# Performance work log

Hardware: AMD Instinct MI355X
Metric: run time of the kernel (lower is better)

The kernel has to match this reference:

```python
import jax, jax.numpy as jnp
import numpy as np

B, S, E, H = 4, 2048, 2048, 16
HD = E // H  # 128
SCALE = 1.0 / float(np.sqrt(HD))


def setup_inputs() -> dict:
    key = jax.random.key(0)
    ks = jax.random.split(key, 9)
    std = 0.02
    return {
        "QKV": jax.random.normal(ks[0], (B, S, E), dtype=jnp.float32),
        "Wq": jax.random.normal(ks[1], (E, E), dtype=jnp.float32) * std,
        "bq": jnp.zeros((E,), dtype=jnp.float32),
        "Wk": jax.random.normal(ks[2], (E, E), dtype=jnp.float32) * std,
        "bk": jnp.zeros((E,), dtype=jnp.float32),
        "Wv": jax.random.normal(ks[3], (E, E), dtype=jnp.float32) * std,
        "bv": jnp.zeros((E,), dtype=jnp.float32),
        "Wo": jax.random.normal(ks[4], (E, E), dtype=jnp.float32) * std,
        "bo": jnp.zeros((E,), dtype=jnp.float32),
        "is_causal": 1,
    }


def _split_heads(x):
    # [B,S,E] -> [B,H,S,HD]
    return x.reshape(B, -1, H, HD).transpose(0, 2, 1, 3)


def reference(QKV, Wq, bq, Wk, bk, Wv, bv, Wo, bo, is_causal):
    # nn.Linear: y = x @ W.T + b
    Q = _split_heads(QKV @ Wq.T + bq)
    K = _split_heads(QKV @ Wk.T + bk)
    V = _split_heads(QKV @ Wv.T + bv)
    P = jnp.einsum("bhqd,bhkd->bhqk", Q, K) * SCALE
    # FAITHFUL: original masked_fill uses (ones_like(...) == 0) -> all-False
    # mask, so causal masking is a no-op regardless of is_causal.
    P = jax.nn.softmax(P, axis=-1)
    out = jnp.einsum("bhqk,bhkd->bhqd", P, V)
    out = out.transpose(0, 2, 1, 3).reshape(B, -1, E)  # [B,S,E]
    return out @ Wo.T + bo
```

## Files before the change

### kernel.cpp

```cpp
#include <hip/hip_runtime.h>
#include <stdint.h>

#define BB 4
#define SS 2048
#define EE 2048
#define HH 16
#define HD 128
#define SCALE 0.08838834764831845f

typedef __attribute__((ext_vector_type(8))) short bf16x8;
typedef __attribute__((ext_vector_type(4))) float f32x4;

__device__ __forceinline__ unsigned short f2bf(float f) {
  union { float f; unsigned u; } v;
  v.f = f;
  unsigned r = (v.u + 0x7fffu + ((v.u >> 16) & 1u)) >> 16;
  return (unsigned short)r;
}
__device__ __forceinline__ float bf2f(unsigned short u) {
  union { unsigned u; float f; } v;
  v.u = ((unsigned)u) << 16;
  return v.f;
}

__device__ __forceinline__ void lds16(const void* g, void* l) {
  __builtin_amdgcn_global_load_lds(
      (__attribute__((address_space(1))) void*)(uintptr_t)g,
      (__attribute__((address_space(3))) void*)(uintptr_t)l,
      16, 0, 0);
}

__global__ void cvt_f32_bf16(const float* __restrict__ src,
                             unsigned short* __restrict__ dst, int n4) {
  int i = blockIdx.x * blockDim.x + threadIdx.x;
  if (i >= n4) return;
  float4 v = ((const float4*)src)[i];
  ushort4 o;
  o.x = f2bf(v.x); o.y = f2bf(v.y); o.z = f2bf(v.z); o.w = f2bf(v.w);
  ((ushort4*)dst)[i] = o;
}

__device__ __forceinline__ void gemm_bt_core(const unsigned short* __restrict__ A,
                                             const unsigned short* __restrict__ Bm,
                                             unsigned short* As, unsigned short* Bs,
                                             int m0, int n0, int K, f32x4 acc[4][4]) {
  const int t = threadIdx.x;
  const int w = t >> 6;
  const int lr = t & 15;
  const int lg = (t & 63) >> 4;
  const int wm = (w >> 1) * 64;
  const int wn = (w & 1) * 64;

  const unsigned short* Ag0 = A + (size_t)(m0 + (t >> 2)) * K + (t & 3) * 8;
  const unsigned short* Ag1 = Ag0 + (size_t)64 * K;
  const unsigned short* Bg0 = Bm + (size_t)(n0 + (t >> 2)) * K + (t & 3) * 8;
  const unsigned short* Bg1 = Bg0 + (size_t)64 * K;
  char* AsB = (char*)As + (w * 64) * 16;
  char* BsB = (char*)Bs + (w * 64) * 16;

#pragma unroll
  for (int i = 0; i < 4; ++i)
#pragma unroll
    for (int j = 0; j < 4; ++j)
      acc[i][j] = (f32x4){0.f, 0.f, 0.f, 0.f};

  for (int kt = 0; kt < K; kt += 32) {
    lds16(Ag0 + kt, AsB);
    lds16(Ag1 + kt, AsB + 256 * 16);
    lds16(Bg0 + kt, BsB);
    lds16(Bg1 + kt, BsB + 256 * 16);
    __syncthreads();
    bf16x8 af[4], bf[4];
#pragma unroll
    for (int i = 0; i < 4; ++i)
      af[i] = *(const bf16x8*)(As + (wm + i * 16 + lr) * 32 + lg * 8);
#pragma unroll
    for (int j = 0; j < 4; ++j)
      bf[j] = *(const bf16x8*)(Bs + (wn + j * 16 + lr) * 32 + lg * 8);
#pragma unroll
    for (int i = 0; i < 4; ++i)
#pragma unroll
      for (int j = 0; j < 4; ++j)
        acc[i][j] = __builtin_amdgcn_mfma_f32_16x16x32_bf16(af[i], bf[j], acc[i][j], 0, 0, 0);
    __syncthreads();
  }
}

__global__ __launch_bounds__(256, 2)
void gemm_qkv(const unsigned short* __restrict__ X,
              const unsigned short* __restrict__ W,
              const float* __restrict__ bq,
              const float* __restrict__ bk,
              const float* __restrict__ bv,
              unsigned short* __restrict__ Qb,
              unsigned short* __restrict__ Kb,
              unsigned short* __restrict__ Vb) {
  __shared__ __align__(16) unsigned short As[128 * 32];
  __shared__ __align__(16) unsigned short Bs[128 * 32];
  const int m0 = blockIdx.y * 128;
  const int n0 = blockIdx.x * 128;
  f32x4 acc[4][4];
  gemm_bt_core(X, W, As, Bs, m0, n0, EE, acc);

  const int t = threadIdx.x;
  const int w = t >> 6;
  const int lr = t & 15;
  const int lg = (t & 63) >> 4;
  const int wm = (w >> 1) * 64;
  const int wn = (w & 1) * 64;

  const int region = n0 >> 11;
  unsigned short* Dst = (region == 0) ? Qb : (region == 1) ? Kb : Vb;
  const float* bp = (region == 0) ? bq : (region == 1) ? bk : bv;

  if (region == 2) {
#pragma unroll
    for (int i = 0; i < 4; ++i) {
      const int row0 = m0 + wm + i * 16 + lg * 4;
      const int b = row0 >> 11;
      const int s = row0 & 2047;
#pragma unroll
      for (int j = 0; j < 4; ++j) {
        const int c = (n0 + wn + j * 16 + lr) & 2047;
        const float bias = bp[c];
        const int h = c >> 7, hd = c & 127;
        const size_t base = ((size_t)(b * HH + h) * HD + hd) * SS + s;
#pragma unroll
        for (int re = 0; re < 4; ++re)
          Dst[base + re] = f2bf(acc[i][j][re] + bias);
      }
    }
  } else {
#pragma unroll
    for (int i = 0; i < 4; ++i) {
      const int row0 = m0 + wm + i * 16 + lg * 4;
      const int b = row0 >> 11;
      const int s = row0 & 2047;
#pragma unroll
      for (int j = 0; j < 4; ++j) {
        const int c = (n0 + wn + j * 16 + lr) & 2047;
        const float bias = bp[c];
        const int h = c >> 7, hd = c & 127;
        const size_t base = ((size_t)(b * HH + h) * SS + s) * HD + hd;
#pragma unroll
        for (int re = 0; re < 4; ++re)
          Dst[base + (size_t)re * HD] = f2bf(acc[i][j][re] + bias);
      }
    }
  }
}

__global__ __launch_bounds__(256, 2)
void gemm_out(const unsigned short* __restrict__ A,
              const unsigned short* __restrict__ W,
              const float* __restrict__ bo,
              float* __restrict__ Out) {
  __shared__ __align__(16) unsigned short As[128 * 32];
  __shared__ __align__(16) unsigned short Bs[128 * 32];
  const int m0 = blockIdx.y * 128;
  const int n0 = blockIdx.x * 128;
  f32x4 acc[4][4];
  gemm_bt_core(A, W, As, Bs, m0, n0, EE, acc);

  const int t = threadIdx.x;
  const int w = t >> 6;
  const int lr = t & 15;
  const int lg = (t & 63) >> 4;
  const int wm = (w >> 1) * 64;
  const int wn = (w & 1) * 64;

#pragma unroll
  for (int i = 0; i < 4; ++i) {
    const int row0 = m0 + wm + i * 16 + lg * 4;
#pragma unroll
    for (int j = 0; j < 4; ++j) {
      const int col = n0 + wn + j * 16 + lr;
      const float bias = bo[col];
#pragma unroll
      for (int re = 0; re < 4; ++re)
        Out[(size_t)(row0 + re) * EE + col] = acc[i][j][re] + bias;
    }
  }
}

__global__ __launch_bounds__(256, 2)
void attn_mfma(const unsigned short* __restrict__ Qb,
               const unsigned short* __restrict__ Kb,
               const unsigned short* __restrict__ Vtb,
               unsigned short* __restrict__ At) {
  __shared__ __align__(16) char lds[49152];
  char* Ks = lds;
  char* Vs = lds + 16384;
  const int t = threadIdx.x;
  const int w = t >> 6;
  const int ln = t & 63;
  const int lr = ln & 15;
  const int lg = ln >> 4;
  char* Ps = lds + 32768 + w * 4096;

  const int bh = blockIdx.y;
  const int qw = blockIdx.x * 128 + w * 32;

  const unsigned short* Qh = Qb + (size_t)bh * SS * HD;
  const unsigned short* Kh = Kb + (size_t)bh * SS * HD;
  const unsigned short* Vh = Vtb + (size_t)bh * HD * SS;

  bf16x8 qfr[2][4];
#pragma unroll
  for (int qi = 0; qi < 2; ++qi)
#pragma unroll
    for (int ds = 0; ds < 4; ++ds)
      qfr[qi][ds] = *(const bf16x8*)(Qh + (size_t)(qw + qi * 16 + lr) * HD + ds * 32 + lg * 8);

  f32x4 acc[8][2];
#pragma unroll
  for (int df = 0; df < 8; ++df)
#pragma unroll
    for (int qi = 0; qi < 2; ++qi)
      acc[df][qi] = (f32x4){0.f, 0.f, 0.f, 0.f};
  float mrun[2] = {-1e30f, -1e30f};
  float lsum[2] = {0.f, 0.f};

  for (int kt = 0; kt < SS; kt += 64) {
#pragma unroll
    for (int i = 0; i < 4; ++i) {
      const int c = i * 256 + w * 64 + ln;
      const int row = c >> 4;
      const int gch = (c & 15) ^ (row & 7);
      lds16(Kh + (size_t)(kt + row) * HD + gch * 8, Ks + (i * 256 + w * 64) * 16);
    }
#pragma unroll
    for (int i = 0; i < 4; ++i) {
      const int c = i * 256 + w * 64 + ln;
      const int d = c >> 3;
      const int kc = (c & 7) ^ (d & 7);
      lds16(Vh + (size_t)d * SS + kt + kc * 8, Vs + (i * 256 + w * 64) * 16);
    }
    __syncthreads();

    f32x4 st[4][2];
#pragma unroll
    for (int kf = 0; kf < 4; ++kf) {
#pragma unroll
      for (int qi = 0; qi < 2; ++qi) st[kf][qi] = (f32x4){0.f, 0.f, 0.f, 0.f};
#pragma unroll
      for (int ds = 0; ds < 4; ++ds) {
        const int krow = kf * 16 + lr;
        bf16x8 kfr = *(const bf16x8*)(Ks + krow * 256 + (((ds * 4 + lg) ^ (krow & 7)) * 16));
#pragma unroll
        for (int qi = 0; qi < 2; ++qi)
          st[kf][qi] = __builtin_amdgcn_mfma_f32_16x16x32_bf16(kfr, qfr[qi][ds], st[kf][qi], 0, 0, 0);
      }
    }

#pragma unroll
    for (int qi = 0; qi < 2; ++qi) {
      float tm = st[0][qi][0];
#pragma unroll
      for (int kf = 0; kf < 4; ++kf)
#pragma unroll
        for (int r = 0; r < 4; ++r) tm = fmaxf(tm, st[kf][qi][r]);
      tm = fmaxf(tm, __shfl_xor(tm, 16, 64));
      tm = fmaxf(tm, __shfl_xor(tm, 32, 64));
      const float mnew = fmaxf(mrun[qi], tm);
      const float alpha = __expf((mrun[qi] - mnew) * SCALE);
      mrun[qi] = mnew;
      float rs = 0.f;
      const int qrow = qi * 16 + lr;
#pragma unroll
      for (int kf = 0; kf < 4; ++kf) {
        const float p0 = __expf((st[kf][qi][0] - mnew) * SCALE);
        const float p1 = __expf((st[kf][qi][1] - mnew) * SCALE);
        const float p2 = __expf((st[kf][qi][2] - mnew) * SCALE);
        const float p3 = __expf((st[kf][qi][3] - mnew) * SCALE);
        rs += (p0 + p1) + (p2 + p3);
        ushort4 pk;
        pk.x = f2bf(p0); pk.y = f2bf(p1); pk.z = f2bf(p2); pk.w = f2bf(p3);
        const int k0 = kf * 16 + lg * 4;
        *(ushort4*)(Ps + qrow * 128 + (((k0 >> 3) ^ (qrow & 7)) * 16) + (k0 & 7) * 2) = pk;
      }
      lsum[qi] = lsum[qi] * alpha + rs;
#pragma unroll
      for (int df = 0; df < 8; ++df) {
        acc[df][qi][0] *= alpha; acc[df][qi][1] *= alpha;
        acc[df][qi][2] *= alpha; acc[df][qi][3] *= alpha;
      }
    }

    bf16x8 pf[2][2];
#pragma unroll
    for (int ks = 0; ks < 2; ++ks)
#pragma unroll
      for (int qi = 0; qi < 2; ++qi) {
        const int qrow = qi * 16 + lr;
        pf[ks][qi] = *(const bf16x8*)(Ps + qrow * 128 + (((ks * 4 + lg) ^ (qrow & 7)) * 16));
      }
#pragma unroll
    for (int df = 0; df < 8; ++df) {
#pragma unroll
      for (int ks = 0; ks < 2; ++ks) {
        const int drow = df * 16 + lr;
        bf16x8 vfr = *(const bf16x8*)(Vs + drow * 128 + (((ks * 4 + lg) ^ (drow & 7)) * 16));
#pragma unroll
        for (int qi = 0; qi < 2; ++qi)
          acc[df][qi] = __builtin_amdgcn_mfma_f32_16x16x32_bf16(vfr, pf[ks][qi], acc[df][qi], 0, 0, 0);
      }
    }
    __syncthreads();
  }

  const int b = bh >> 4, h = bh & 15;
#pragma unroll
  for (int qi = 0; qi < 2; ++qi) {
    float l = lsum[qi];
    l += __shfl_xor(l, 16, 64);
    l += __shfl_xor(l, 32, 64);
    const float rl = 1.0f / l;
    const int s = qw + qi * 16 + lr;
    unsigned short* orow = At + ((size_t)(b * SS + s)) * EE + h * HD;
#pragma unroll
    for (int df = 0; df < 8; ++df)
#pragma unroll
      for (int r = 0; r < 4; ++r)
        orow[df * 16 + lg * 4 + r] = f2bf(acc[df][qi][r] * rl);
  }
}

extern "C" void kernel_launch(void* const* d_in, const int* in_sizes, int n_in,
                              void* d_out, int out_size, void* d_ws, size_t ws_size,
                              hipStream_t stream) {
  const float* QKV = (const float*)d_in[0];
  const float* Wq  = (const float*)d_in[1];
  const float* bq  = (const float*)d_in[2];
  const float* Wk  = (const float*)d_in[3];
  const float* bk  = (const float*)d_in[4];
  const float* Wv  = (const float*)d_in[5];
  const float* bv  = (const float*)d_in[6];
  const float* Wo  = (const float*)d_in[7];
  const float* bo  = (const float*)d_in[8];

  unsigned short* Xb = (unsigned short*)d_out;

  char* ws = (char*)d_ws;
  unsigned short* Wqkvb = (unsigned short*)(ws);
  unsigned short* Qb    = (unsigned short*)(ws + ( 24u << 20));
  unsigned short* Kb    = (unsigned short*)(ws + ( 56u << 20));
  unsigned short* Vb    = (unsigned short*)(ws + ( 88u << 20));
  unsigned short* At    = (unsigned short*)(ws + (120u << 20));
  unsigned short* Wob   = Wqkvb;

  cvt_f32_bf16<<<dim3(16384), dim3(256), 0, stream>>>(QKV, Xb, 4194304);
  cvt_f32_bf16<<<dim3(4096), dim3(256), 0, stream>>>(Wq, Wqkvb, 1048576);
  cvt_f32_bf16<<<dim3(4096), dim3(256), 0, stream>>>(Wk, Wqkvb + 4194304, 1048576);
  cvt_f32_bf16<<<dim3(4096), dim3(256), 0, stream>>>(Wv, Wqkvb + 8388608, 1048576);

  gemm_qkv<<<dim3(48, 64), dim3(256), 0, stream>>>(Xb, Wqkvb, bq, bk, bv, Qb, Kb, Vb);
  attn_mfma<<<dim3(16, 64), dim3(256), 0, stream>>>(Qb, Kb, Vb, At);

  cvt_f32_bf16<<<dim3(4096), dim3(256), 0, stream>>>(Wo, Wob, 1048576);
  gemm_out<<<dim3(16, 64), dim3(256), 0, stream>>>(At, Wob, bo, (float*)d_out);
}
```

Baseline: 684.1 us.

## Double-buffer K/V in attention, fold softmax scale into Q, lazy rescale, merge weight casts

The attention kernel now stages the next K/V tile into a second LDS buffer while computing on the current one, removing one barrier per iteration. The softmax scale and log2(e) are folded into Q at projection time so the kernel can use exp2 directly. Rescaling of the running accumulator is skipped unless the row max grows by more than a threshold, and MFMA sections get raised wave priority. The three weight-conversion launches are merged into one. The larger LDS footprint (80KB) may reduce occupancy, and lazy rescaling lets unnormalized values grow up to 2^8 before a rescale.

```diff
diff --git a/kernel.cpp b/kernel.cpp
--- a/kernel.cpp
+++ b/kernel.cpp
@@ -6,7 +6,7 @@
 #define EE 2048
 #define HH 16
 #define HD 128
-#define SCALE 0.08838834764831845f
+#define QSCALE 0.1275174490044696f
 
 typedef __attribute__((ext_vector_type(8))) short bf16x8;
 typedef __attribute__((ext_vector_type(4))) float f32x4;
@@ -38,6 +38,21 @@
   ushort4 o;
   o.x = f2bf(v.x); o.y = f2bf(v.y); o.z = f2bf(v.z); o.w = f2bf(v.w);
   ((ushort4*)dst)[i] = o;
+}
+
+__global__ void cvt_w3(const float* __restrict__ Wq,
+                       const float* __restrict__ Wk,
+                       const float* __restrict__ Wv,
+                       unsigned short* __restrict__ dst, int n4each) {
+  const int which = blockIdx.y;
+  const float* src = (which == 0) ? Wq : (which == 1) ? Wk : Wv;
+  unsigned short* d = dst + (size_t)which * 4194304;
+  int i = blockIdx.x * blockDim.x + threadIdx.x;
+  if (i >= n4each) return;
+  float4 v = ((const float4*)src)[i];
+  ushort4 o;
+  o.x = f2bf(v.x); o.y = f2bf(v.y); o.z = f2bf(v.z); o.w = f2bf(v.w);
+  ((ushort4*)d)[i] = o;
 }
 
 __device__ __forceinline__ void gemm_bt_core(const unsigned short* __restrict__ A,
@@ -131,6 +146,7 @@
       }
     }
   } else {
+    const float osc = (region == 0) ? QSCALE : 1.0f;
 #pragma unroll
     for (int i = 0; i < 4; ++i) {
       const int row0 = m0 + wm + i * 16 + lg * 4;
@@ -144,7 +160,7 @@
         const size_t base = ((size_t)(b * HH + h) * SS + s) * HD + hd;
 #pragma unroll
         for (int re = 0; re < 4; ++re)
-          Dst[base + (size_t)re * HD] = f2bf(acc[i][j][re] + bias);
+          Dst[base + (size_t)re * HD] = f2bf((acc[i][j][re] + bias) * osc);
       }
     }
   }
@@ -188,15 +204,13 @@
                const unsigned short* __restrict__ Kb,
                const unsigned short* __restrict__ Vtb,
                unsigned short* __restrict__ At) {
-  __shared__ __align__(16) char lds[49152];
-  char* Ks = lds;
-  char* Vs = lds + 16384;
+  __shared__ __align__(16) char lds[81920];
   const int t = threadIdx.x;
   const int w = t >> 6;
   const int ln = t & 63;
   const int lr = ln & 15;
   const int lg = ln >> 4;
-  char* Ps = lds + 32768 + w * 4096;
+  char* Ps = lds + 65536 + w * 4096;
 
   const int bh = blockIdx.y;
   const int qw = blockIdx.x * 128 + w * 32;
@@ -218,27 +232,41 @@
 #pragma unroll
     for (int qi = 0; qi < 2; ++qi)
       acc[df][qi] = (f32x4){0.f, 0.f, 0.f, 0.f};
-  float mrun[2] = {-1e30f, -1e30f};
+  float mrun[2] = {-3.0e38f, -3.0e38f};
   float lsum[2] = {0.f, 0.f};
 
+#define STAGE_KV(kt, buf)                                                      \
+  do {                                                                         \
+    char* Kd = lds + (buf) * 32768;                                            \
+    char* Vd = Kd + 16384;                                                     \
+    _Pragma("unroll") for (int i = 0; i < 4; ++i) {                            \
+      const int c = i * 256 + w * 64 + ln;                                     \
+      const int row = c >> 4;                                                  \
+      const int gch = (c & 15) ^ (row & 7);                                    \
+      lds16(Kh + (size_t)((kt) + row) * HD + gch * 8,                          \
+            Kd + (i * 256 + w * 64) * 16);                                     \
+    }                                                                          \
+    _Pragma("unroll") for (int i = 0; i < 4; ++i) {                            \
+      const int c = i * 256 + w * 64 + ln;                                     \
+      const int d = c >> 3;                                                    \
+      const int kc = (c & 7) ^ (d & 7);                                        \
+      lds16(Vh + (size_t)d * SS + (kt) + kc * 8,                               \
+            Vd + (i * 256 + w * 64) * 16);                                     \
+    }                                                                          \
+  } while (0)
+
+  STAGE_KV(0, 0);
+  __syncthreads();
+
+  int cur = 0;
   for (int kt = 0; kt < SS; kt += 64) {
-#pragma unroll
-    for (int i = 0; i < 4; ++i) {
-      const int c = i * 256 + w * 64 + ln;
-      const int row = c >> 4;
-      const int gch = (c & 15) ^ (row & 7);
-      lds16(Kh + (size_t)(kt + row) * HD + gch * 8, Ks + (i * 256 + w * 64) * 16);
-    }
-#pragma unroll
-    for (int i = 0; i < 4; ++i) {
-      const int c = i * 256 + w * 64 + ln;
-      const int d = c >> 3;
-      const int kc = (c & 7) ^ (d & 7);
-      lds16(Vh + (size_t)d * SS + kt + kc * 8, Vs + (i * 256 + w * 64) * 16);
-    }
-    __syncthreads();
+    if (kt + 64 < SS) STAGE_KV(kt + 64, cur ^ 1);
+
+    char* Ks = lds + cur * 32768;
+    char* Vs = Ks + 16384;
 
     f32x4 st[4][2];
+    __builtin_amdgcn_s_setprio(1);
 #pragma unroll
     for (int kf = 0; kf < 4; ++kf) {
 #pragma unroll
@@ -252,6 +280,7 @@
           st[kf][qi] = __builtin_amdgcn_mfma_f32_16x16x32_bf16(kfr, qfr[qi][ds], st[kf][qi], 0, 0, 0);
       }
     }
+    __builtin_amdgcn_s_setprio(0);
 
 #pragma unroll
     for (int qi = 0; qi < 2; ++qi) {
@@ -262,29 +291,33 @@
         for (int r = 0; r < 4; ++r) tm = fmaxf(tm, st[kf][qi][r]);
       tm = fmaxf(tm, __shfl_xor(tm, 16, 64));
       tm = fmaxf(tm, __shfl_xor(tm, 32, 64));
-      const float mnew = fmaxf(mrun[qi], tm);
-      const float alpha = __expf((mrun[qi] - mnew) * SCALE);
-      mrun[qi] = mnew;
+      if (!__all(tm <= mrun[qi] + 8.0f)) {
+        const float mnew = fmaxf(mrun[qi], tm);
+        const float alpha = __builtin_exp2f(mrun[qi] - mnew);
+        mrun[qi] = mnew;
+        lsum[qi] *= alpha;
+#pragma unroll
+        for (int df = 0; df < 8; ++df) {
+          acc[df][qi][0] *= alpha; acc[df][qi][1] *= alpha;
+          acc[df][qi][2] *= alpha; acc[df][qi][3] *= alpha;
+        }
+      }
+      const float mcur = mrun[qi];
       float rs = 0.f;
       const int qrow = qi * 16 + lr;
 #pragma unroll
       for (int kf = 0; kf < 4; ++kf) {
-        const float p0 = __expf((st[kf][qi][0] - mnew) * SCALE);
-        const float p1 = __expf((st[kf][qi][1] - mnew) * SCALE);
-        const float p2 = __expf((st[kf][qi][2] - mnew) * SCALE);
-        const float p3 = __expf((st[kf][qi][3] - mnew) * SCALE);
+        const float p0 = __builtin_exp2f(st[kf][qi][0] - mcur);
+        const float p1 = __builtin_exp2f(st[kf][qi][1] - mcur);
+        const float p2 = __builtin_exp2f(st[kf][qi][2] - mcur);
+        const float p3 = __builtin_exp2f(st[kf][qi][3] - mcur);
         rs += (p0 + p1) + (p2 + p3);
         ushort4 pk;
         pk.x = f2bf(p0); pk.y = f2bf(p1); pk.z = f2bf(p2); pk.w = f2bf(p3);
         const int k0 = kf * 16 + lg * 4;
         *(ushort4*)(Ps + qrow * 128 + (((k0 >> 3) ^ (qrow & 7)) * 16) + (k0 & 7) * 2) = pk;
       }
-      lsum[qi] = lsum[qi] * alpha + rs;
-#pragma unroll
-      for (int df = 0; df < 8; ++df) {
-        acc[df][qi][0] *= alpha; acc[df][qi][1] *= alpha;
-        acc[df][qi][2] *= alpha; acc[df][qi][3] *= alpha;
-      }
+      lsum[qi] += rs;
     }
 
     bf16x8 pf[2][2];
@@ -295,6 +328,7 @@
         const int qrow = qi * 16 + lr;
         pf[ks][qi] = *(const bf16x8*)(Ps + qrow * 128 + (((ks * 4 + lg) ^ (qrow & 7)) * 16));
       }
+    __builtin_amdgcn_s_setprio(1);
 #pragma unroll
     for (int df = 0; df < 8; ++df) {
 #pragma unroll
@@ -306,7 +340,10 @@
           acc[df][qi] = __builtin_amdgcn_mfma_f32_16x16x32_bf16(vfr, pf[ks][qi], acc[df][qi], 0, 0, 0);
       }
     }
+    __builtin_amdgcn_s_setprio(0);
+
     __syncthreads();
+    cur ^= 1;
   }
 
   const int b = bh >> 4, h = bh & 15;
@@ -350,9 +387,7 @@
   unsigned short* Wob   = Wqkvb;
 
   cvt_f32_bf16<<<dim3(16384), dim3(256), 0, stream>>>(QKV, Xb, 4194304);
-  cvt_f32_bf16<<<dim3(4096), dim3(256), 0, stream>>>(Wq, Wqkvb, 1048576);
-  cvt_f32_bf16<<<dim3(4096), dim3(256), 0, stream>>>(Wk, Wqkvb + 4194304, 1048576);
-  cvt_f32_bf16<<<dim3(4096), dim3(256), 0, stream>>>(Wv, Wqkvb + 8388608, 1048576);
+  cvt_w3<<<dim3(4096, 3), dim3(256), 0, stream>>>(Wq, Wk, Wv, Wqkvb, 1048576);
 
   gemm_qkv<<<dim3(48, 64), dim3(256), 0, stream>>>(Xb, Wqkvb, bq, bk, bv, Qb, Kb, Vb);
   attn_mfma<<<dim3(16, 64), dim3(256), 0, stream>>>(Qb, Kb, Vb, At);
```

After: 676.8 us. About the same (-1.1%).
